# Kernel tuning notes

Measured on AMD Instinct MI355X. Metric: run time of the kernel, lower is better.

The kernel has to match this reference:

```python
import jax, jax.numpy as jnp
import numpy as np

B, N, F_IN, HID, HEADS, LAYERS = 512, 128, 128, 64, 4, 3
NEG_SLOPE = 0.2  # DenseGATConv default


def setup_inputs() -> dict:
    key = jax.random.key(0)
    ks = jax.random.split(key, 1 + 4 * LAYERS)
    inp = {}
    inp["x"] = jax.random.normal(ks[0], (B * N, F_IN), jnp.float32)
    # uniform graph sizes: graph i owns nodes [i*N, (i+1)*N)
    inp["batch_mask"] = jnp.repeat(jnp.arange(B, dtype=jnp.int32), N)
    dims = [F_IN] + [HID * HEADS] * (LAYERS - 1)
    for l in range(LAYERS):
        d = dims[l]
        k = 4 * l
        inp[f"W{l}"] = jax.random.normal(ks[1 + k], (d, HEADS * HID), jnp.float32) / np.sqrt(d)
        inp[f"att_src{l}"] = jax.random.normal(ks[2 + k], (HEADS, HID), jnp.float32) * 0.1
        inp[f"att_dst{l}"] = jax.random.normal(ks[3 + k], (HEADS, HID), jnp.float32) * 0.1
        inp[f"b{l}"] = jnp.zeros((HEADS * HID,), jnp.float32)  # zero-init bias, as in PyG
    return inp


def _dense_gat(x, adj, W, att_src, att_dst, bias):
    # x: [B, N, F_in], adj: [N, N] (shared structure, broadcast over batch)
    b, n, _ = x.shape
    h = (x @ W).reshape(b, n, HEADS, HID)                       # [B,N,H,C]
    a_src = jnp.einsum('bnhc,hc->bnh', h, att_src)              # [B,N,H]
    a_dst = jnp.einsum('bnhc,hc->bnh', h, att_dst)              # [B,N,H]
    # alpha[b,i,j,h] = a_src[b,j,h] + a_dst[b,i,h]
    alpha = a_src[:, None, :, :] + a_dst[:, :, None, :]         # [B,N,N,H]
    alpha = jnp.where(alpha >= 0, alpha, NEG_SLOPE * alpha)
    alpha = jnp.where(adj[None, :, :, None] == 0, -jnp.inf, alpha)
    alpha = jax.nn.softmax(alpha, axis=2)                       # softmax over sources j
    out = jnp.einsum('bijh,bjhc->bihc', alpha, h)               # [B,N,H,C]
    return out.reshape(b, n, HEADS * HID) + bias                # concat heads + bias


def reference(x, batch_mask, W0, att_src0, att_dst0, b0,
              W1, att_src1, att_dst1, b1, W2, att_src2, att_dst2, b2):
    # to_dense_batch with uniform graph sizes == reshape; batch_mask encodes this layout
    h = x.reshape(B, N, F_IN)
    eye = jnp.eye(N, dtype=x.dtype)
    # GNNBlock builds full adjacency with zeroed diagonal ...
    adj = jnp.ones((N, N), x.dtype) - eye
    # ... and DenseGATConv(add_loop=True) re-adds self-loops
    adj = jnp.maximum(adj, eye)
    params = [(W0, att_src0, att_dst0, b0), (W1, att_src1, att_dst1, b1),
              (W2, att_src2, att_dst2, b2)]
    for (W, a_s, a_d, b) in params:
        h = _dense_gat(h, adj, W, a_s, a_d, b)
        # block act is nn.LeakyReLU(True): negative_slope=True==1.0 -> identity
        h = jnp.where(h >= 0, h, 1.0 * h)
    return h.sum(axis=1)  # [B, HEADS*HID]
```

## Files before the change

kernel.cpp:

```cpp
#include <hip/hip_runtime.h>
#include <hip/hip_bf16.h>


typedef unsigned short u16;
typedef __attribute__((ext_vector_type(8))) short short8;
typedef __attribute__((ext_vector_type(4))) float f32x4;

#define L2E 1.44269504088896340736f

__device__ __forceinline__ u16 f2bf(float f) {
  unsigned int u = __float_as_uint(f);
  u += 0x7fffu + ((u >> 16) & 1u);
  return (u16)(u >> 16);
}
__device__ __forceinline__ unsigned int pk2(float a, float b) {
  __hip_bfloat162 h2 = __float22bfloat162_rn(make_float2(a, b));
  unsigned int u;
  __builtin_memcpy(&u, &h2, 4);
  return u;
}

__device__ __forceinline__ int xs_byte(int row, int col) {
  return (row << 9) + ((col << 1) ^ ((row & 7) << 4));
}
__device__ __forceinline__ int ht_byte(int row, int col) {
  return (row << 8) + ((col << 1) ^ ((row & 7) << 4));
}

__global__ void prep_w(const float* __restrict__ W0, const float* __restrict__ W1,
                       const float* __restrict__ W2,
                       const float* __restrict__ as0, const float* __restrict__ ad0,
                       const float* __restrict__ as1, const float* __restrict__ ad1,
                       const float* __restrict__ as2, const float* __restrict__ ad2,
                       u16* __restrict__ wt) {
  int gid = blockIdx.x * 256 + threadIdx.x;
  if (gid < 163840) {
    const float* W; int nkb, base;
    if (gid < 32768)      { W = W0; nkb = 4; base = 0; }
    else if (gid < 98304) { W = W1; nkb = 8; base = 32768; }
    else                  { W = W2; nkb = 8; base = 98304; }
    int idx  = gid - base;
    int e    = idx & 7;
    int lane = (idx >> 3) & 63;
    int rest = idx >> 9;
    int t = rest / nkb, kb = rest - t * nkb;
    int n = t * 16 + (lane & 15);
    int k = kb * 32 + (lane >> 4) * 8 + e;
    wt[gid] = f2bf(W[k * 256 + n]);
  } else if (gid < 174080) {
    int idx = gid - 163840;
    const float* W; const float* as; const float* ad; int base2;
    if (idx < 2048)      { W = W0; as = as0; ad = ad0; base2 = 0; }
    else if (idx < 6144) { W = W1; as = as1; ad = ad1; base2 = 2048; }
    else                 { W = W2; as = as2; ad = ad2; base2 = 6144; }
    int i2 = idx - base2;
    int e = i2 & 7, lane = (i2 >> 3) & 63, kb = i2 >> 9;
    int l15 = lane & 15;
    int k = kb * 32 + (lane >> 4) * 8 + e;
    float v = 0.f;
    if (l15 < 8) {
      const float* av = (l15 < 4) ? as : ad;
      int h = l15 & 3;
      for (int c = 0; c < 64; ++c)
        v = fmaf(W[k * 256 + h * 64 + c], av[h * 64 + c], v);
    }
    wt[gid] = f2bf(v);
  }
}

__global__ __launch_bounds__(1024, 4) void gat_all(
    const float* __restrict__ x, const u16* __restrict__ wt,
    const float* __restrict__ bb0, const float* __restrict__ bb1,
    const float* __restrict__ bb2, float* __restrict__ out)
{
  constexpr int XS = 0;
  constexpr int HT = 65536;
  constexpr int SB = 131072;
  constexpr int DB = 133120;
  constexpr int ML = 135168;
  constexpr int PT = 137216;
  constexpr int PM = 141312;
  constexpr int BS = 141440;
  constexpr int OA = 142464;
  __shared__ unsigned char smem[143488];

  float* sbuf  = (float*)(smem + SB);
  float* dbuf  = (float*)(smem + DB);
  float* mlb   = (float*)(smem + ML);
  float* ptmp  = (float*)(smem + PT);
  float* pmaxw = (float*)(smem + PM);
  float* bsb   = (float*)(smem + BS);
  float* oac   = (float*)(smem + OA);

  const int b    = blockIdx.x;
  const int tid  = threadIdx.x;
  const int w    = tid >> 6;
  const int lane = tid & 63;
  const int l15  = lane & 15;
  const int lg   = lane >> 4;

  {
    const float4* xg = (const float4*)(x + (size_t)b * (128 * 128));
    #pragma unroll
    for (int it = 0; it < 4; ++it) {
      int e = tid + it * 1024;
      float4 v = xg[e];
      int row = e >> 5, c = (e & 31) << 2;
      uint2 u = { pk2(v.x, v.y), pk2(v.z, v.w) };
      *(uint2*)(smem + XS + xs_byte(row, c)) = u;
    }
  }
  __syncthreads();

  const u16* wfl[3]   = {wt, wt + 32768, wt + 98304};
  const u16* wsdp[3]  = {wt + 163840, wt + 165888, wt + 169984};
  const float* bias[3] = {bb0, bb1, bb2};

  #pragma unroll
  for (int l = 0; l < 3; ++l) {
    const int NKB = (l == 0) ? 4 : 8;

    if (tid < 256) bsb[tid] = bias[l][tid];
    {
      const int mw = w & 1, nw = w >> 1;
      f32x4 acc[4][2] = {};
      const u16* wf = wfl[l];
      #pragma unroll
      for (int ks = 0; ks < NKB; ++ks) {
        const int kcol = ks * 32 + lg * 8;
        short8 afr[4];
        #pragma unroll
        for (int mi = 0; mi < 4; ++mi)
          afr[mi] = *(const short8*)(smem + XS + xs_byte(mw * 64 + mi * 16 + l15, kcol));
        short8 bfr[2];
        #pragma unroll
        for (int ni = 0; ni < 2; ++ni) {
          int t = nw * 2 + ni;
          bfr[ni] = *(const short8*)(wf + (((t * NKB + ks) * 64 + lane) << 3));
        }
        #pragma unroll
        for (int mi = 0; mi < 4; ++mi)
          #pragma unroll
          for (int ni = 0; ni < 2; ++ni)
            acc[mi][ni] = __builtin_amdgcn_mfma_f32_16x16x32_bf16(
                afr[mi], bfr[ni], acc[mi][ni], 0, 0, 0);
      }
      #pragma unroll
      for (int mi = 0; mi < 4; ++mi) {
        int j0 = mw * 64 + mi * 16 + lg * 4;
        #pragma unroll
        for (int ni = 0; ni < 2; ++ni) {
          int c = nw * 32 + ni * 16 + l15;
          uint2 u = { pk2(acc[mi][ni][0], acc[mi][ni][1]),
                      pk2(acc[mi][ni][2], acc[mi][ni][3]) };
          *(uint2*)(smem + HT + ht_byte(c, j0)) = u;
        }
      }
    }
    __syncthreads();

    if (w < 8) {
      f32x4 acc = {};
      const u16* wv = wsdp[l];
      #pragma unroll
      for (int ks = 0; ks < NKB; ++ks) {
        int kcol = ks * 32 + lg * 8;
        short8 a = *(const short8*)(smem + XS + xs_byte(w * 16 + l15, kcol));
        short8 bq = *(const short8*)(wv + ((ks * 64 + lane) << 3));
        acc = __builtin_amdgcn_mfma_f32_16x16x32_bf16(a, bq, acc, 0, 0, 0);
      }
      if (l15 < 8) {
        float* basep = (float*)(smem + (l15 < 4 ? SB : DB)) + (l15 & 3) * 128 + w * 16 + lg * 4;
        *(float4*)basep = (float4){acc[0], acc[1], acc[2], acc[3]};
      }
      float m = fmaxf(fmaxf(acc[0], acc[1]), fmaxf(acc[2], acc[3]));
      m = fmaxf(m, __shfl_xor(m, 16));
      m = fmaxf(m, __shfl_xor(m, 32));
      if (lg == 0 && l15 < 4) pmaxw[l15 * 8 + w] = m;
    }
    __syncthreads();

    {
      int p = tid & 511, half = tid >> 9;
      int h = p >> 7;
      float smax = pmaxw[h * 8];
      #pragma unroll
      for (int q2 = 1; q2 < 8; ++q2) smax = fmaxf(smax, pmaxw[h * 8 + q2]);
      float dv = dbuf[p];
      float mlr = smax + dv;
      mlr = fmaxf(mlr, 0.2f * mlr);
      float ml = mlr * L2E;
      const float* sr = sbuf + h * 128 + half * 64;
      float den0 = 0.f, den1 = 0.f;
      #pragma unroll 8
      for (int jj = 0; jj < 64; jj += 2) {
        float va = sr[jj] + dv, vb = sr[jj + 1] + dv;
        va = fmaxf(va, 0.2f * va);
        vb = fmaxf(vb, 0.2f * vb);
        den0 += exp2f(fmaf(va, L2E, -ml));
        den1 += exp2f(fmaf(vb, L2E, -ml));
      }
      ptmp[half * 512 + p] = den0 + den1;
      if (half == 0) mlb[p] = ml;
      if (l == 2 && tid < 256) oac[tid] = 0.f;
    }
    __syncthreads();

    {
      const int hw = w >> 2, q = w & 3;
      f32x4 acc[4][2] = {};
      float dvv[2], mlv[2];
      int iblk[2];
      #pragma unroll
      for (int ni = 0; ni < 2; ++ni) {
        int i = q * 32 + ni * 16 + l15;
        iblk[ni] = hw * 128 + i;
        dvv[ni] = dbuf[iblk[ni]];
        mlv[ni] = mlb[iblk[ni]];
      }
      #pragma unroll
      for (int ks = 0; ks < 4; ++ks) {
        const int j0 = ks * 32 + lg * 8;
        float sj[8];
        #pragma unroll
        for (int jj = 0; jj < 8; ++jj) sj[jj] = sbuf[hw * 128 + j0 + jj];
        short8 afr[4];
        #pragma unroll
        for (int mi = 0; mi < 4; ++mi)
          afr[mi] = *(const short8*)(smem + HT + ht_byte(hw * 64 + mi * 16 + l15, j0));
        short8 bfr[2];
        #pragma unroll
        for (int ni = 0; ni < 2; ++ni) {
          float e[8];
          #pragma unroll
          for (int jj = 0; jj < 8; ++jj) {
            float v = sj[jj] + dvv[ni];
            v = fmaxf(v, 0.2f * v);
            e[jj] = exp2f(fmaf(v, L2E, -mlv[ni]));
          }
          union { short8 s; unsigned int u[4]; } pk;
          #pragma unroll
          for (int t2 = 0; t2 < 4; ++t2) pk.u[t2] = pk2(e[2 * t2], e[2 * t2 + 1]);
          bfr[ni] = pk.s;
        }
        #pragma unroll
        for (int mi = 0; mi < 4; ++mi)
          #pragma unroll
          for (int ni = 0; ni < 2; ++ni)
            acc[mi][ni] = __builtin_amdgcn_mfma_f32_16x16x32_bf16(
                afr[mi], bfr[ni], acc[mi][ni], 0, 0, 0);
      }
      float rvv[2];
      #pragma unroll
      for (int ni = 0; ni < 2; ++ni)
        rvv[ni] = 1.f / (ptmp[iblk[ni]] + ptmp[512 + iblk[ni]]);
      if (l < 2) {
        #pragma unroll
        for (int mi = 0; mi < 4; ++mi) {
          int c0 = hw * 64 + mi * 16 + lg * 4;
          float b0v = bsb[c0], b1v = bsb[c0 + 1], b2v = bsb[c0 + 2], b3v = bsb[c0 + 3];
          #pragma unroll
          for (int ni = 0; ni < 2; ++ni) {
            int i = q * 32 + ni * 16 + l15;
            float r = rvv[ni];
            uint2 u = { pk2(fmaf(acc[mi][ni][0], r, b0v), fmaf(acc[mi][ni][1], r, b1v)),
                        pk2(fmaf(acc[mi][ni][2], r, b2v), fmaf(acc[mi][ni][3], r, b3v)) };
            *(uint2*)(smem + XS + xs_byte(i, c0)) = u;
          }
        }
      } else {
        #pragma unroll
        for (int mi = 0; mi < 4; ++mi) {
          #pragma unroll
          for (int reg = 0; reg < 4; ++reg) {
            float pv2 = acc[mi][0][reg] * rvv[0] + acc[mi][1][reg] * rvv[1];
            pv2 += __shfl_xor(pv2, 1);
            pv2 += __shfl_xor(pv2, 2);
            pv2 += __shfl_xor(pv2, 4);
            pv2 += __shfl_xor(pv2, 8);
            if (l15 == 0)
              atomicAdd(&oac[hw * 64 + mi * 16 + lg * 4 + reg], pv2);
          }
        }
      }
    }
    __syncthreads();
  }

  if (tid < 256) out[(size_t)b * 256 + tid] = oac[tid] + 128.f * bsb[tid];
}

extern "C" void kernel_launch(void* const* d_in, const int* in_sizes, int n_in,
                              void* d_out, int out_size, void* d_ws, size_t ws_size,
                              hipStream_t stream) {
  const float* x   = (const float*)d_in[0];
  const float* W0  = (const float*)d_in[2];
  const float* as0 = (const float*)d_in[3];
  const float* ad0 = (const float*)d_in[4];
  const float* b0  = (const float*)d_in[5];
  const float* W1  = (const float*)d_in[6];
  const float* as1 = (const float*)d_in[7];
  const float* ad1 = (const float*)d_in[8];
  const float* b1  = (const float*)d_in[9];
  const float* W2  = (const float*)d_in[10];
  const float* as2 = (const float*)d_in[11];
  const float* ad2 = (const float*)d_in[12];
  const float* b2  = (const float*)d_in[13];
  u16* wt = (u16*)d_ws;

  hipLaunchKernelGGL(prep_w, dim3(680), dim3(256), 0, stream,
                     W0, W1, W2, as0, ad0, as1, ad1, as2, ad2, wt);
  hipLaunchKernelGGL(gat_all, dim3(512), dim3(1024), 0, stream,
                     x, wt, b0, b1, b2, (float*)d_out);
}
```

Measured before the change: 207.3 us.

## Fuse attention-score GEMM and softmax denominator into main GEMM phases

Appends the src/dst attention projection as an extra N-tile of the packed weight layout. Two spare waves (14 and 15) compute it alongside the main feature GEMM, which removes one barrier phase and prescales the scores by log2(e). The separate softmax-denominator pass is removed: denominators are accumulated from the same exp values used for the aggregation MFMA and then reduced with cross-lane shuffles, which drops two more barriers and some shared buffers. The weight-prep kernel is also rewritten to use far fewer blocks with vectorized 16-byte stores. A risk is load imbalance, since the two extra waves do additional MFMA work while the other waves wait at the barrier.

```diff
diff --git a/kernel.cpp b/kernel.cpp
--- a/kernel.cpp
+++ b/kernel.cpp
@@ -33,38 +33,37 @@
                        const float* __restrict__ as1, const float* __restrict__ ad1,
                        const float* __restrict__ as2, const float* __restrict__ ad2,
                        u16* __restrict__ wt) {
-  int gid = blockIdx.x * 256 + threadIdx.x;
-  if (gid < 163840) {
-    const float* W; int nkb, base;
-    if (gid < 32768)      { W = W0; nkb = 4; base = 0; }
-    else if (gid < 98304) { W = W1; nkb = 8; base = 32768; }
-    else                  { W = W2; nkb = 8; base = 98304; }
-    int idx  = gid - base;
-    int e    = idx & 7;
-    int lane = (idx >> 3) & 63;
-    int rest = idx >> 9;
-    int t = rest / nkb, kb = rest - t * nkb;
-    int n = t * 16 + (lane & 15);
-    int k = kb * 32 + (lane >> 4) * 8 + e;
-    wt[gid] = f2bf(W[k * 256 + n]);
-  } else if (gid < 174080) {
-    int idx = gid - 163840;
-    const float* W; const float* as; const float* ad; int base2;
-    if (idx < 2048)      { W = W0; as = as0; ad = ad0; base2 = 0; }
-    else if (idx < 6144) { W = W1; as = as1; ad = ad1; base2 = 2048; }
-    else                 { W = W2; as = as2; ad = ad2; base2 = 6144; }
-    int i2 = idx - base2;
-    int e = i2 & 7, lane = (i2 >> 3) & 63, kb = i2 >> 9;
-    int l15 = lane & 15;
-    int k = kb * 32 + (lane >> 4) * 8 + e;
-    float v = 0.f;
-    if (l15 < 8) {
-      const float* av = (l15 < 4) ? as : ad;
-      int h = l15 & 3;
-      for (int c = 0; c < 64; ++c)
-        v = fmaf(W[k * 256 + h * 64 + c], av[h * 64 + c], v);
-    }
-    wt[gid] = f2bf(v);
+  const int bid = blockIdx.x, tid = threadIdx.x;
+  if (bid < 80) {
+    const float* W; int NKB, base, rel;
+    if (bid < 16)      { W = W0; NKB = 4; base = 0;      rel = bid; }
+    else if (bid < 48) { W = W1; NKB = 8; base = 34816;  rel = bid - 16; }
+    else               { W = W2; NKB = 8; base = 104448; rel = bid - 48; }
+    const int kb = rel >> 2, ko = rel & 3;
+    const int n = tid;
+    union { u16 v[8]; short8 s; } u;
+    #pragma unroll
+    for (int e = 0; e < 8; ++e)
+      u.v[e] = f2bf(W[(kb * 32 + ko * 8 + e) * 256 + n]);
+    const int t = n >> 4, l15 = n & 15;
+    *(short8*)(wt + base + (((t * NKB + kb) * 64 + l15 + (ko << 4)) << 3)) = u.s;
+  } else if (bid < 100) {
+    int b2 = bid - 80;
+    const float* W; const float* as; const float* ad; int NKB, base, kb;
+    if (b2 < 4)       { W = W0; as = as0; ad = ad0; NKB = 4; base = 0;      kb = b2; }
+    else if (b2 < 12) { W = W1; as = as1; ad = ad1; NKB = 8; base = 34816;  kb = b2 - 4; }
+    else              { W = W2; as = as2; ad = ad2; NKB = 8; base = 104448; kb = b2 - 12; }
+    const int kloc = tid >> 3, col = tid & 7, h = col & 3;
+    const int k = kb * 32 + kloc;
+    const float* av = (col < 4) ? as : ad;
+    float acc = 0.f;
+    #pragma unroll 8
+    for (int c = 0; c < 64; ++c)
+      acc = fmaf(W[k * 256 + h * 64 + c], av[h * 64 + c], acc);
+    const int lane2 = col + ((kloc >> 3) << 4), e = kloc & 7;
+    const int tb = base + ((16 * NKB + kb) << 9);
+    wt[tb + ((lane2) << 3) + e]     = f2bf(acc);
+    wt[tb + ((lane2 + 8) << 3) + e] = 0;
   }
 }
 
@@ -77,17 +76,13 @@
   constexpr int HT = 65536;
   constexpr int SB = 131072;
   constexpr int DB = 133120;
-  constexpr int ML = 135168;
-  constexpr int PT = 137216;
-  constexpr int PM = 141312;
-  constexpr int BS = 141440;
-  constexpr int OA = 142464;
-  __shared__ unsigned char smem[143488];
+  constexpr int PM = 135168;
+  constexpr int BS = 135232;
+  constexpr int OA = 136256;
+  __shared__ unsigned char smem[137280];
 
   float* sbuf  = (float*)(smem + SB);
   float* dbuf  = (float*)(smem + DB);
-  float* mlb   = (float*)(smem + ML);
-  float* ptmp  = (float*)(smem + PT);
   float* pmaxw = (float*)(smem + PM);
   float* bsb   = (float*)(smem + BS);
   float* oac   = (float*)(smem + OA);
@@ -112,20 +107,21 @@
   }
   __syncthreads();
 
-  const u16* wfl[3]   = {wt, wt + 32768, wt + 98304};
-  const u16* wsdp[3]  = {wt + 163840, wt + 165888, wt + 169984};
+  const u16* wfl[3]    = {wt, wt + 34816, wt + 104448};
   const float* bias[3] = {bb0, bb1, bb2};
 
   #pragma unroll
   for (int l = 0; l < 3; ++l) {
     const int NKB = (l == 0) ? 4 : 8;
-
-    if (tid < 256) bsb[tid] = bias[l][tid];
+    const u16* wf = wfl[l];
+
+    if (tid < 256) {
+      bsb[tid] = bias[l][tid];
+      if (l == 2) oac[tid] = 0.f;
+    }
     {
       const int mw = w & 1, nw = w >> 1;
       f32x4 acc[4][2] = {};
-      const u16* wf = wfl[l];
-      #pragma unroll
       for (int ks = 0; ks < NKB; ++ks) {
         const int kcol = ks * 32 + lg * 8;
         short8 afr[4];
@@ -157,66 +153,50 @@
         }
       }
     }
-    __syncthreads();
-
-    if (w < 8) {
-      f32x4 acc = {};
-      const u16* wv = wsdp[l];
-      #pragma unroll
+
+    if (w >= 14) {
+      const int mw = w & 1;
+      f32x4 acc2[4] = {};
       for (int ks = 0; ks < NKB; ++ks) {
-        int kcol = ks * 32 + lg * 8;
-        short8 a = *(const short8*)(smem + XS + xs_byte(w * 16 + l15, kcol));
-        short8 bq = *(const short8*)(wv + ((ks * 64 + lane) << 3));
-        acc = __builtin_amdgcn_mfma_f32_16x16x32_bf16(a, bq, acc, 0, 0, 0);
-      }
-      if (l15 < 8) {
-        float* basep = (float*)(smem + (l15 < 4 ? SB : DB)) + (l15 & 3) * 128 + w * 16 + lg * 4;
-        *(float4*)basep = (float4){acc[0], acc[1], acc[2], acc[3]};
-      }
-      float m = fmaxf(fmaxf(acc[0], acc[1]), fmaxf(acc[2], acc[3]));
-      m = fmaxf(m, __shfl_xor(m, 16));
-      m = fmaxf(m, __shfl_xor(m, 32));
-      if (lg == 0 && l15 < 4) pmaxw[l15 * 8 + w] = m;
-    }
-    __syncthreads();
-
-    {
-      int p = tid & 511, half = tid >> 9;
-      int h = p >> 7;
-      float smax = pmaxw[h * 8];
-      #pragma unroll
-      for (int q2 = 1; q2 < 8; ++q2) smax = fmaxf(smax, pmaxw[h * 8 + q2]);
-      float dv = dbuf[p];
-      float mlr = smax + dv;
-      mlr = fmaxf(mlr, 0.2f * mlr);
-      float ml = mlr * L2E;
-      const float* sr = sbuf + h * 128 + half * 64;
-      float den0 = 0.f, den1 = 0.f;
-      #pragma unroll 8
-      for (int jj = 0; jj < 64; jj += 2) {
-        float va = sr[jj] + dv, vb = sr[jj + 1] + dv;
-        va = fmaxf(va, 0.2f * va);
-        vb = fmaxf(vb, 0.2f * vb);
-        den0 += exp2f(fmaf(va, L2E, -ml));
-        den1 += exp2f(fmaf(vb, L2E, -ml));
-      }
-      ptmp[half * 512 + p] = den0 + den1;
-      if (half == 0) mlb[p] = ml;
-      if (l == 2 && tid < 256) oac[tid] = 0.f;
+        const int kcol = ks * 32 + lg * 8;
+        short8 bsd = *(const short8*)(wf + (((16 * NKB + ks) * 64 + lane) << 3));
+        #pragma unroll
+        for (int mi = 0; mi < 4; ++mi) {
+          short8 a = *(const short8*)(smem + XS + xs_byte(mw * 64 + mi * 16 + l15, kcol));
+          acc2[mi] = __builtin_amdgcn_mfma_f32_16x16x32_bf16(a, bsd, acc2[mi], 0, 0, 0);
+        }
+      }
+      float mx = -3.4e38f;
+      #pragma unroll
+      for (int mi = 0; mi < 4; ++mi) {
+        f32x4 v = acc2[mi] * L2E;
+        if (l15 < 8) {
+          float* basep = (float*)(smem + (l15 < 4 ? SB : DB))
+                       + (l15 & 3) * 128 + mw * 64 + mi * 16 + lg * 4;
+          *(float4*)basep = (float4){v[0], v[1], v[2], v[3]};
+        }
+        mx = fmaxf(mx, fmaxf(fmaxf(v[0], v[1]), fmaxf(v[2], v[3])));
+      }
+      mx = fmaxf(mx, __shfl_xor(mx, 16));
+      mx = fmaxf(mx, __shfl_xor(mx, 32));
+      if (lane < 4) pmaxw[lane * 2 + mw] = mx;
     }
     __syncthreads();
 
     {
       const int hw = w >> 2, q = w & 3;
       f32x4 acc[4][2] = {};
-      float dvv[2], mlv[2];
-      int iblk[2];
+      float den[2] = {0.f, 0.f};
+      float dvv[2], nml[2];
+      int ib[2];
+      const float smax = fmaxf(pmaxw[hw * 2], pmaxw[hw * 2 + 1]);
       #pragma unroll
       for (int ni = 0; ni < 2; ++ni) {
         int i = q * 32 + ni * 16 + l15;
-        iblk[ni] = hw * 128 + i;
-        dvv[ni] = dbuf[iblk[ni]];
-        mlv[ni] = mlb[iblk[ni]];
+        ib[ni] = hw * 128 + i;
+        dvv[ni] = dbuf[ib[ni]];
+        float tm = smax + dvv[ni];
+        nml[ni] = -fmaxf(tm, 0.2f * tm);
       }
       #pragma unroll
       for (int ks = 0; ks < 4; ++ks) {
@@ -234,10 +214,11 @@
           float e[8];
           #pragma unroll
           for (int jj = 0; jj < 8; ++jj) {
-            float v = sj[jj] + dvv[ni];
-            v = fmaxf(v, 0.2f * v);
-            e[jj] = exp2f(fmaf(v, L2E, -mlv[ni]));
+            float t = sj[jj] + dvv[ni];
+            t = fmaxf(t, 0.2f * t);
+            e[jj] = exp2f(t + nml[ni]);
           }
+          den[ni] += ((e[0] + e[1]) + (e[2] + e[3])) + ((e[4] + e[5]) + (e[6] + e[7]));
           union { short8 s; unsigned int u[4]; } pk;
           #pragma unroll
           for (int t2 = 0; t2 < 4; ++t2) pk.u[t2] = pk2(e[2 * t2], e[2 * t2 + 1]);
@@ -252,8 +233,12 @@
       }
       float rvv[2];
       #pragma unroll
-      for (int ni = 0; ni < 2; ++ni)
-        rvv[ni] = 1.f / (ptmp[iblk[ni]] + ptmp[512 + iblk[ni]]);
+      for (int ni = 0; ni < 2; ++ni) {
+        float d2 = den[ni];
+        d2 += __shfl_xor(d2, 16);
+        d2 += __shfl_xor(d2, 32);
+        rvv[ni] = 1.f / d2;
+      }
       if (l < 2) {
         #pragma unroll
         for (int mi = 0; mi < 4; ++mi) {
@@ -308,7 +293,7 @@
   const float* b2  = (const float*)d_in[13];
   u16* wt = (u16*)d_ws;
 
-  hipLaunchKernelGGL(prep_w, dim3(680), dim3(256), 0, stream,
+  hipLaunchKernelGGL(prep_w, dim3(100), dim3(256), 0, stream,
                      W0, W1, W2, as0, ad0, as1, ad1, as2, ad2, wt);
   hipLaunchKernelGGL(gat_all, dim3(512), dim3(1024), 0, stream,
                      x, wt, b0, b1, b2, (float*)d_out);
```

Result: faster. 174.4 us (-15.9%).
